# Kernel tuning notes

Measured on AMD Instinct MI355X. Metric: run time of the kernel, lower is better.

The kernel has to match this reference:

```python
import jax, jax.numpy as jnp
import numpy as np

WIDTH_POW = 9
WIDTH = 2 ** WIDTH_POW          # 512
HALF = WIDTH // 2               # 256
DEPTH = 32
BATCH = 65536
EPS = 0.01


def setup_inputs() -> dict:
    key = jax.random.key(0)
    k1, k2, k3, k4, k5, k6 = jax.random.split(key, 6)
    X = jax.random.normal(k1, (BATCH, WIDTH), dtype=jnp.float32)
    # butterfly rotation angles, one stage of depth-1 butterfly per layer
    thetas = jax.random.uniform(k2, (DEPTH, HALF), dtype=jnp.float32) * (2.0 * np.pi)
    # SmoothBendActivation params, init uniform in [-eps, eps]
    def u(k):
        return jax.random.uniform(k, (DEPTH, WIDTH), dtype=jnp.float32) * (2 * EPS) - EPS
    biases = u(k3)
    slopes1 = u(k4)
    slopes2 = u(k5)
    curvatures = u(k6)
    return {"X": X, "thetas": thetas, "biases": biases,
            "slopes1": slopes1, "slopes2": slopes2, "curvatures": curvatures}


def reference(X, thetas, biases, slopes1, slopes2, curvatures):
    B = X.shape[0]

    def step(x, p):
        theta, bias, s1, s2, curv = p
        # --- orthogonal butterfly rotation (depth 1) ---
        c = jnp.cos(theta)  # [HALF]
        s = jnp.sin(theta)
        x0 = x[:, :HALF]
        x1 = x[:, HALF:]
        n0 = x0 * c + x1 * s
        n1 = -x0 * s + x1 * c
        # fixed permutation perm[2j] = j, perm[2j+1] = j + HALF: interleave n0, n1
        x = jnp.stack([n0, n1], axis=-1).reshape(B, WIDTH)
        # --- smooth bend activation ---
        m1 = jnp.exp(s1)
        m2 = jnp.exp(s2)
        a = (m1 + m2) * 0.5
        cc = (m2 - m1) / (2.0 * a)
        b = jnp.sinh(bias)
        k = jnp.exp(curv)
        u = x * a - b
        x = u + cc * jnp.sqrt(u * u + 1.0 / k)
        return x, None

    out, _ = jax.lax.scan(step, X, (thetas, biases, slopes1, slopes2, curvatures))
    return out  # num_outputs == WIDTH, so no final slice needed
```

## Files before the change

kernel.cpp:

```cpp
#include <hip/hip_runtime.h>
#include <math.h>

#define WIDTH 512
#define HALF  256
#define DEPTH 32
#define BATCH 65536
#define RPW   8
#define NS    4

__device__ float4 g_T1[DEPTH * WIDTH];
__device__ float  g_T2[DEPTH * WIDTH];

__global__ __launch_bounds__(256) void precompute_kernel(
    const float* __restrict__ thetas, const float* __restrict__ biases,
    const float* __restrict__ slopes1, const float* __restrict__ slopes2,
    const float* __restrict__ curvatures) {
  int tid = blockIdx.x * 256 + threadIdx.x;
  if (tid >= DEPTH * WIDTH) return;
  int d = tid >> 9;
  int idx = tid & 511;
  int w = idx >> 8, s = (idx >> 6) & 3, l = idx & 63;
  int p = w * 256 + l * 4 + s;
  int rot = (d + 1) % 9;
  int j = ((p << rot) | (p >> (9 - rot))) & 511;
  int i = j >> 1;
  int role = j & 1;
  float th = thetas[d * HALF + i];
  float c = cosf(th), sn = sinf(th);
  float m1 = expf(slopes1[d * WIDTH + j]);
  float m2 = expf(slopes2[d * WIDTH + j]);
  float a  = 0.5f * (m1 + m2);
  float cc = (m2 - m1) / (m1 + m2);
  float b  = sinhf(biases[d * WIDTH + j]);
  float ik = expf(-curvatures[d * WIDTH + j]);
  float A = a * c;
  float S = role ? (-a * sn) : (a * sn);
  g_T1[d * WIDTH + idx] = make_float4(A, S, b, cc);
  g_T2[d * WIDTH + idx] = ik;
}

#if __has_builtin(__builtin_amdgcn_sqrtf)
#define FAST_SQRT(x) __builtin_amdgcn_sqrtf(x)
#else
#define FAST_SQRT(x) sqrtf(x)
#endif

template <int M>
__device__ __forceinline__ float xshfl(float v) {
  if constexpr (M < 32) {
    constexpr int ctl = (M << 10) | 0x1F;
    return __int_as_float(__builtin_amdgcn_ds_swizzle(__float_as_int(v), ctl));
  } else {
    return __shfl_xor(v, 32, 64);
  }
}

__device__ __forceinline__ float stepf(float xs, float v, float4 P, float ik) {
  float u = fmaf(xs, P.x, fmaf(v, P.y, -P.z));
  float t = fmaf(u, u, ik);
  return fmaf(P.w, FAST_SQRT(t), u);
}

template <int K>
__device__ __forceinline__ void layer_step(const float4* __restrict__ t1,
                                           const float* __restrict__ t2,
                                           float (&x)[NS][RPW], float* xb,
                                           int tid) {
  if constexpr (K == 8) {
#pragma unroll
    for (int s = 0; s < NS; ++s)
#pragma unroll
      for (int r = 0; r < RPW; ++r)
        xb[(s * RPW + r) * 128 + tid] = x[s][r];
    __syncthreads();
    const int pt = tid ^ 64;
#pragma unroll
    for (int s = 0; s < NS; ++s) {
      float4 P = t1[s * 64];
      float ik = t2[s * 64];
      float v[RPW];
#pragma unroll
      for (int r = 0; r < RPW; ++r) v[r] = xb[(s * RPW + r) * 128 + pt];
#pragma unroll
      for (int r = 0; r < RPW; ++r) x[s][r] = stepf(x[s][r], v[r], P, ik);
    }
    __syncthreads();
  } else if constexpr (K >= 2) {
    constexpr int m = 1 << (K - 2);
#pragma unroll
    for (int s = 0; s < NS; ++s) {
      float4 P = t1[s * 64];
      float ik = t2[s * 64];
#pragma unroll
      for (int r = 0; r < RPW; ++r) {
        float xs = x[s][r];
        float v = xshfl<m>(xs);
        x[s][r] = stepf(xs, v, P, ik);
      }
    }
  } else {
    constexpr int SX = 1 << K;
#pragma unroll
    for (int s0 = 0; s0 < NS; ++s0) {
      if (s0 & SX) continue;
      const int s1 = s0 | SX;
      float4 P0 = t1[s0 * 64];
      float ik0 = t2[s0 * 64];
      float4 P1 = t1[s1 * 64];
      float ik1 = t2[s1 * 64];
#pragma unroll
      for (int r = 0; r < RPW; ++r) {
        float v0 = x[s0][r], v1 = x[s1][r];
        float n0 = stepf(v0, v1, P0, ik0);
        float n1 = stepf(v1, v0, P1, ik1);
        x[s0][r] = n0;
        x[s1][r] = n1;
      }
    }
  }
}

__global__ __launch_bounds__(128, 4) void net_kernel(const float* __restrict__ X,
                                                     float* __restrict__ out) {
  __shared__ float xb[NS * RPW * 128];
  const int tid = threadIdx.x;
  const int lane = tid & 63;
  const int w = tid >> 6;
  const size_t row0 = (size_t)blockIdx.x * RPW;

  float x[NS][RPW];
  const float* __restrict__ Xp = X + row0 * WIDTH + w * 256 + lane * 4;
#pragma unroll
  for (int r = 0; r < RPW; ++r) {
    float4 a = *reinterpret_cast<const float4*>(Xp + (size_t)r * WIDTH);
    x[0][r] = a.x; x[1][r] = a.y; x[2][r] = a.z; x[3][r] = a.w;
  }

  const int poff = w * 256 + lane;
#define RUN_LAYER(DD)                                                    \
  do {                                                                   \
    if (d0 + DD < DEPTH) {                                               \
      layer_step<8 - DD>(g_T1 + (d0 + DD) * WIDTH + poff,                \
                         g_T2 + (d0 + DD) * WIDTH + poff, x, xb, tid);   \
    }                                                                    \
  } while (0)

#pragma unroll 1
  for (int d0 = 0; d0 < DEPTH; d0 += 9) {
    RUN_LAYER(0); RUN_LAYER(1); RUN_LAYER(2);
    RUN_LAYER(3); RUN_LAYER(4); RUN_LAYER(5);
    RUN_LAYER(6); RUN_LAYER(7); RUN_LAYER(8);
  }
#undef RUN_LAYER

  float* __restrict__ O = out + row0 * WIDTH;
#pragma unroll
  for (int s = 0; s < NS; ++s) {
    const int p = w * 256 + lane * 4 + s;
    const int cfin = ((p << 5) | (p >> 4)) & 511;
#pragma unroll
    for (int r = 0; r < RPW; ++r) O[r * WIDTH + cfin] = x[s][r];
  }
}

extern "C" void kernel_launch(void* const* d_in, const int* in_sizes, int n_in,
                              void* d_out, int out_size, void* d_ws, size_t ws_size,
                              hipStream_t stream) {
  const float* X          = (const float*)d_in[0];
  const float* thetas     = (const float*)d_in[1];
  const float* biases     = (const float*)d_in[2];
  const float* slopes1    = (const float*)d_in[3];
  const float* slopes2    = (const float*)d_in[4];
  const float* curvatures = (const float*)d_in[5];
  float* out = (float*)d_out;

  hipLaunchKernelGGL(precompute_kernel, dim3((DEPTH * WIDTH + 255) / 256),
                     dim3(256), 0, stream, thetas, biases, slopes1, slopes2,
                     curvatures);
  hipLaunchKernelGGL(net_kernel, dim3(BATCH / RPW), dim3(128), 0, stream,
                     X, out);
}
```

Measured before the change: 201.6 us.

## Prefetch next layer's parameters in registers and halve the LDS exchange buffer

Each layer now loads the following layer's per-lane parameters into registers while computing with the ones loaded one step earlier, so global parameter-load latency is hidden behind the arithmetic. The cross-wave LDS exchange is split into two chunks of two slices, which cuts shared memory per block from 16KB to 8KB but adds extra barriers. The parameter tables grow by one depth row so the final prefetch stays in bounds; that row is never written, and its values are loaded but not used. Prefetching costs extra registers, which could reduce occupancy.

```diff
diff --git a/kernel.cpp b/kernel.cpp
--- a/kernel.cpp
+++ b/kernel.cpp
@@ -8,8 +8,8 @@
 #define RPW   8
 #define NS    4
 
-__device__ float4 g_T1[DEPTH * WIDTH];
-__device__ float  g_T2[DEPTH * WIDTH];
+__device__ float4 g_T1[(DEPTH + 1) * WIDTH];
+__device__ float  g_T2[(DEPTH + 1) * WIDTH];
 
 __global__ __launch_bounds__(256) void precompute_kernel(
     const float* __restrict__ thetas, const float* __restrict__ biases,
@@ -62,40 +62,50 @@
 }
 
 template <int K>
-__device__ __forceinline__ void layer_step(const float4* __restrict__ t1,
-                                           const float* __restrict__ t2,
-                                           float (&x)[NS][RPW], float* xb,
-                                           int tid) {
+__device__ __forceinline__ void layer_step(const float4* __restrict__ t1n,
+                                           const float* __restrict__ t2n,
+                                           float (&x)[NS][RPW],
+                                           float4 (&P)[NS], float (&IK)[NS],
+                                           float* xb, int tid) {
+  float4 cur[NS];
+  float cik[NS];
+#pragma unroll
+  for (int s = 0; s < NS; ++s) {
+    cur[s] = P[s];
+    cik[s] = IK[s];
+    P[s] = t1n[s * 64];
+    IK[s] = t2n[s * 64];
+  }
+
   if constexpr (K == 8) {
-#pragma unroll
-    for (int s = 0; s < NS; ++s)
-#pragma unroll
-      for (int r = 0; r < RPW; ++r)
-        xb[(s * RPW + r) * 128 + tid] = x[s][r];
-    __syncthreads();
     const int pt = tid ^ 64;
 #pragma unroll
-    for (int s = 0; s < NS; ++s) {
-      float4 P = t1[s * 64];
-      float ik = t2[s * 64];
-      float v[RPW];
+    for (int c = 0; c < NS; c += 2) {
 #pragma unroll
-      for (int r = 0; r < RPW; ++r) v[r] = xb[(s * RPW + r) * 128 + pt];
+      for (int s = c; s < c + 2; ++s)
 #pragma unroll
-      for (int r = 0; r < RPW; ++r) x[s][r] = stepf(x[s][r], v[r], P, ik);
+        for (int r = 0; r < RPW; ++r)
+          xb[((s - c) * RPW + r) * 128 + tid] = x[s][r];
+      __syncthreads();
+#pragma unroll
+      for (int s = c; s < c + 2; ++s) {
+        float v[RPW];
+#pragma unroll
+        for (int r = 0; r < RPW; ++r) v[r] = xb[((s - c) * RPW + r) * 128 + pt];
+#pragma unroll
+        for (int r = 0; r < RPW; ++r) x[s][r] = stepf(x[s][r], v[r], cur[s], cik[s]);
+      }
+      __syncthreads();
     }
-    __syncthreads();
   } else if constexpr (K >= 2) {
     constexpr int m = 1 << (K - 2);
 #pragma unroll
     for (int s = 0; s < NS; ++s) {
-      float4 P = t1[s * 64];
-      float ik = t2[s * 64];
 #pragma unroll
       for (int r = 0; r < RPW; ++r) {
         float xs = x[s][r];
         float v = xshfl<m>(xs);
-        x[s][r] = stepf(xs, v, P, ik);
+        x[s][r] = stepf(xs, v, cur[s], cik[s]);
       }
     }
   } else {
@@ -104,15 +114,11 @@
     for (int s0 = 0; s0 < NS; ++s0) {
       if (s0 & SX) continue;
       const int s1 = s0 | SX;
-      float4 P0 = t1[s0 * 64];
-      float ik0 = t2[s0 * 64];
-      float4 P1 = t1[s1 * 64];
-      float ik1 = t2[s1 * 64];
 #pragma unroll
       for (int r = 0; r < RPW; ++r) {
         float v0 = x[s0][r], v1 = x[s1][r];
-        float n0 = stepf(v0, v1, P0, ik0);
-        float n1 = stepf(v1, v0, P1, ik1);
+        float n0 = stepf(v0, v1, cur[s0], cik[s0]);
+        float n1 = stepf(v1, v0, cur[s1], cik[s1]);
         x[s0][r] = n0;
         x[s1][r] = n1;
       }
@@ -122,7 +128,7 @@
 
 __global__ __launch_bounds__(128, 4) void net_kernel(const float* __restrict__ X,
                                                      float* __restrict__ out) {
-  __shared__ float xb[NS * RPW * 128];
+  __shared__ float xb[2 * RPW * 128];
   const int tid = threadIdx.x;
   const int lane = tid & 63;
   const int w = tid >> 6;
@@ -137,12 +143,22 @@
   }
 
   const int poff = w * 256 + lane;
-#define RUN_LAYER(DD)                                                    \
-  do {                                                                   \
-    if (d0 + DD < DEPTH) {                                               \
-      layer_step<8 - DD>(g_T1 + (d0 + DD) * WIDTH + poff,                \
-                         g_T2 + (d0 + DD) * WIDTH + poff, x, xb, tid);   \
-    }                                                                    \
+
+  float4 P[NS];
+  float IK[NS];
+#pragma unroll
+  for (int s = 0; s < NS; ++s) {
+    P[s] = g_T1[poff + s * 64];
+    IK[s] = g_T2[poff + s * 64];
+  }
+
+#define RUN_LAYER(DD)                                                     \
+  do {                                                                    \
+    if (d0 + DD < DEPTH) {                                                \
+      layer_step<8 - DD>(g_T1 + (d0 + DD + 1) * WIDTH + poff,             \
+                         g_T2 + (d0 + DD + 1) * WIDTH + poff,             \
+                         x, P, IK, xb, tid);                              \
+    }                                                                     \
   } while (0)
 
 #pragma unroll 1
```

After: 205.9 us. 2.1% more time.
